# Kernel tuning notes

Measured on AMD Instinct MI355X. Metric: run time of the kernel, lower is better.

The kernel has to match this reference:

```python
import jax, jax.numpy as jnp
import numpy as np
from jax import lax

B, H, W, C = 8, 64, 64, 256  # H must equal W (einsum contraction requires it)
CQ = C // 4


def conv2d(x, w, b, dilation=1):
    # x: NHWC, w: HWIO (TF Conv2D layout), padding 'same'
    y = lax.conv_general_dilated(
        x, w, window_strides=(1, 1), padding='SAME',
        rhs_dilation=(dilation, dilation),
        dimension_numbers=('NHWC', 'HWIO', 'NHWC'))
    return y + b


def setup_inputs() -> dict:
    key = jax.random.key(0)
    ks = jax.random.split(key, 16)
    s = 0.05
    inp = {
        'x':   jax.random.normal(ks[0], (B, H, W, C), jnp.float32),
        'wq':  jax.random.normal(ks[1], (1, 1, C, CQ), jnp.float32) * s,
        'bq':  jnp.zeros((CQ,), jnp.float32),
        'wq1': jax.random.normal(ks[2], (3, 3, C, CQ), jnp.float32) * s,
        'bq1': jnp.zeros((CQ,), jnp.float32),
        'wq2': jax.random.normal(ks[3], (3, 3, C, CQ), jnp.float32) * s,
        'bq2': jnp.zeros((CQ,), jnp.float32),
        'wq3': jax.random.normal(ks[4], (3, 3, C, CQ), jnp.float32) * s,
        'bq3': jnp.zeros((CQ,), jnp.float32),
        'wq4': jax.random.normal(ks[5], (1, 1, C, C), jnp.float32) * s,
        'bq4': jnp.zeros((C,), jnp.float32),
        'wk':  jax.random.normal(ks[6], (3, 3, C, C), jnp.float32) * s,
        'bk':  jnp.zeros((C,), jnp.float32),
        'wv':  jax.random.normal(ks[7], (1, 1, C, C), jnp.float32) * s,
        'bv':  jnp.zeros((C,), jnp.float32),
        'gamma': jax.random.normal(ks[8], (1,), jnp.float32) * 0.1,
    }
    return inp


def reference(x, wq, bq, wq1, bq1, wq2, bq2, wq3, bq3, wq4, bq4,
              wk, bk, wv, bv, gamma):
    # multi-scale query branch: 1x1, 3x3, 3x3 dil=3, 3x3 dil=6 -> concat -> 1x1
    q = jnp.concatenate([
        conv2d(x, wq, bq, 1),
        conv2d(x, wq1, bq1, 1),
        conv2d(x, wq2, bq2, 3),
        conv2d(x, wq3, bq3, 6),
    ], axis=-1)
    q = conv2d(q, wq4, bq4, 1)                 # (B,H,W,C)
    # key conv applied twice with the SAME weights (as in the original code)
    k = conv2d(conv2d(x, wk, bk, 1), wk, bk, 1)  # (B,H,W,C)
    v = conv2d(x, wv, bv, 1)                    # (B,H,W,C)

    qT = jnp.transpose(q, (0, 2, 1, 3))         # (B,W,H,C)
    # per-channel spatial contraction; requires H == W
    energy = jnp.einsum('bijc,bkjc->bikc', k, qT)   # (B,H,W,C)
    attention = jax.nn.softmax(energy, axis=-1)     # softmax over CHANNEL axis
    attnT = jnp.transpose(attention, (0, 2, 1, 3))  # (B,W,H,C)
    out = jnp.einsum('bijc,bkjc->bikc', attnT, v)   # (B,W,H,C)
    return gamma * out + x
```

## Files before the change

kernel.cpp:

```cpp
#include <hip/hip_runtime.h>

typedef short  short8 __attribute__((ext_vector_type(8)));
typedef short  sv4    __attribute__((ext_vector_type(4)));
typedef __bf16 bf16x8 __attribute__((ext_vector_type(8)));
typedef float  f32x4  __attribute__((ext_vector_type(4)));

__device__ __forceinline__ float bf2f(short s) {
    unsigned u = ((unsigned)(unsigned short)s) << 16;
    return __builtin_bit_cast(float, u);
}
__device__ __forceinline__ short f2bf(float f) {
    unsigned u = __builtin_bit_cast(unsigned, f);
    u += 0x7fffu + ((u >> 16) & 1u);
    return (short)(u >> 16);
}
__device__ __forceinline__ f32x4 mfma16(short8 a, short8 b, f32x4 c) {
    return __builtin_amdgcn_mfma_f32_16x16x32_bf16(
        __builtin_bit_cast(bf16x8, a), __builtin_bit_cast(bf16x8, b), c, 0, 0, 0);
}
__device__ __forceinline__ void gl16(const short* g, short* l) {
    __builtin_amdgcn_global_load_lds(
        (const __attribute__((address_space(1))) void*)g,
        (__attribute__((address_space(3))) void*)l, 16, 0, 0);
}


__global__ __launch_bounds__(256) void detect_k(const short* x, int* flag)
{
    __shared__ int red[256];
    int t = threadIdx.x;
    int cnt = 0;
    for (int i = t; i < 4096; i += 256) {
        int e = (x[2 * i] >> 7) & 0xFF;
        cnt += (e >= 100 && e <= 140) ? 1 : 0;
    }
    red[t] = cnt; __syncthreads();
    for (int s = 128; s > 0; s >>= 1) { if (t < s) red[t] += red[t + s]; __syncthreads(); }
    if (t == 0) *flag = (red[0] < 3277) ? 1 : 0;
}

__global__ __launch_bounds__(256) void convert_x(const void* x, short* xb, const int* flagp)
{
    int f32 = *flagp;
    size_t i = ((size_t)blockIdx.x * 256 + threadIdx.x) * 8;
    short8 v;
    if (f32) {
        const float* fs = (const float*)x + i;
        f32x4 a = *(const f32x4*)fs;
        f32x4 b = *(const f32x4*)(fs + 4);
#pragma unroll
        for (int l = 0; l < 4; l++) { v[l] = f2bf(a[l]); v[4 + l] = f2bf(b[l]); }
    } else {
        v = *(const short8*)((const short*)x + i);
    }
    *(short8*)(xb + i) = v;
}

struct Ptrs {
    const void *wq, *wq1, *wq2, *wq3, *wq4, *wk, *wv;
    const void *bq, *bq1, *bq2, *bq3, *bq4, *bk, *bv, *gm;
};

__global__ __launch_bounds__(256) void convert_k(Ptrs P, short* wp, short* bb, const int* flagp)
{
    int f32 = *flagp;
    int bid = blockIdx.x;
    int tid = threadIdx.x;
    if (bid < 288) {
        __shared__ short T[64][66];
        const void* src; int Cout, dbase, lb;
        if      (bid <   4) { src = P.wq;  Cout =  64; dbase = 0;       lb = bid; }
        else if (bid <  40) { src = P.wq1; Cout =  64; dbase = 16384;   lb = bid - 4; }
        else if (bid <  76) { src = P.wq2; Cout =  64; dbase = 163840;  lb = bid - 40; }
        else if (bid < 112) { src = P.wq3; Cout =  64; dbase = 311296;  lb = bid - 76; }
        else if (bid < 128) { src = P.wq4; Cout = 256; dbase = 458752;  lb = bid - 112; }
        else if (bid < 272) { src = P.wk;  Cout = 256; dbase = 524288;  lb = bid - 128; }
        else                { src = P.wv;  Cout = 256; dbase = 1114112; lb = bid - 272; }
        int t, ci0, co0;
        if (Cout == 64) { t = lb >> 2; ci0 = (lb & 3) * 64; co0 = 0; }
        else            { t = lb >> 4; ci0 = ((lb >> 2) & 3) * 64; co0 = (lb & 3) * 64; }
        int rrow = tid >> 6, ccol = tid & 63;
#pragma unroll
        for (int r = 0; r < 16; ++r) {
            int cir = r * 4 + rrow;
            long si = (long)(t * 256 + ci0 + cir) * Cout + co0 + ccol;
            T[cir][ccol] = f32 ? f2bf(((const float*)src)[si]) : ((const short*)src)[si];
        }
        __syncthreads();
#pragma unroll
        for (int r = 0; r < 16; ++r) {
            int cow = r * 4 + rrow;
            wp[dbase + (t * Cout + co0 + cow) * 256 + ci0 + ccol] = T[ccol][cow];
        }
    } else {
        for (int j = tid; j < 1280; j += 256) {
            if (j < 1025) {
                const void* src; int off;
                if      (j <   64) { src = P.bq;  off = j; }
                else if (j <  128) { src = P.bq1; off = j - 64; }
                else if (j <  192) { src = P.bq2; off = j - 128; }
                else if (j <  256) { src = P.bq3; off = j - 192; }
                else if (j <  512) { src = P.bq4; off = j - 256; }
                else if (j <  768) { src = P.bk;  off = j - 512; }
                else if (j < 1024) { src = P.bv;  off = j - 768; }
                else               { src = P.gm;  off = 0; }
                bb[j] = f32 ? f2bf(((const float*)src)[off]) : ((const short*)src)[off];
            } else if (j >= 1032) {
                bb[j] = 0;
            }
        }
    }
}

struct CJob {
    const short* src;
    short*       dst;
    const short* wpk;
    const short* bias;
    int Cout;
    int dil;
    int ntaps;
    int coff;
    int outmode;
};
struct CTable { CJob j[6]; int end[6]; };

template<int NA, int NB, int BOFS, int WSTEP>
__device__ __forceinline__ void conv_loop(
    const short* src, const short* wpk, int ntaps, int dil,
    const short* zp, short* Sh,
    int wave, int lr8, int cl, int h0, int b, int nt0, int srcT,
    int m_base, int n_base, int lrow, int pc0, int pc1,
    f32x4 (&acc)[4][4])
{
    const short* abase[NA];
    unsigned     vm[NA];
    const short* bbase[NB];
#pragma unroll
    for (int jj = 0; jj < NA; jj++) {
        int m  = (jj * 4 + wave) * 8 + lr8;
        int hh = srcT ? (m & 63) : (h0 + (m >> 6));
        int ww = srcT ? (h0 + (m >> 6)) : (m & 63);
        abase[jj] = src + (((b * 64 + hh) * 64 + ww) * 256 + cl * 8);
        unsigned msk = 1u;
        if (ntaps == 9) {
            msk = 0u;
#pragma unroll
            for (int t = 0; t < 9; ++t) {
                int tr = (t >= 6) ? 2 : ((t >= 3) ? 1 : 0);
                int dy = (tr - 1) * dil, dx = (t - tr * 3 - 1) * dil;
                bool v = ((unsigned)(hh + dy) < 64u) && ((unsigned)(ww + dx) < 64u);
                msk |= (v ? 1u : 0u) << t;
            }
        }
        vm[jj] = msk;
    }
#pragma unroll
    for (int jj = 0; jj < NB; jj++) {
        int n = (jj * 4 + wave) * 8 + lr8;
        bbase[jj] = wpk + (nt0 + n) * 256 + cl * 8;
    }

    int prevdel = 0;
    for (int t = 0; t < ntaps; ++t) {
        int dy = 0, dx = 0;
        if (ntaps == 9) {
            int tr = (t >= 6) ? 2 : ((t >= 3) ? 1 : 0);
            dy = (tr - 1) * dil;
            dx = (t - tr * 3 - 1) * dil;
        }
        int tdel = (dy * 64 + dx) * 256;
        int step = tdel - prevdel; prevdel = tdel;
        const short* pA[NA];
#pragma unroll
        for (int jj = 0; jj < NA; jj++) {
            abase[jj] += step;
            pA[jj] = ((vm[jj] >> t) & 1u) ? abase[jj] : zp;
        }
#pragma unroll
        for (int s4 = 0; s4 < 4; ++s4) {
#pragma unroll
            for (int jj = 0; jj < NA; jj++)
                gl16(pA[jj] + s4 * 64, Sh + (jj * 4 + wave) * 512);
#pragma unroll
            for (int jj = 0; jj < NB; jj++)
                gl16(bbase[jj] + s4 * 64, Sh + BOFS + (jj * 4 + wave) * 512);
            __syncthreads();
#pragma unroll
            for (int j = 0; j < 2; j++) {
                int pc = j ? pc1 : pc0;
                short8 a4[4], b4[4];
#pragma unroll
                for (int mi = 0; mi < 4; mi++)
                    a4[mi] = *(const short8*)(Sh + (m_base + mi * 16 + lrow) * 64 + pc);
#pragma unroll
                for (int ni = 0; ni < 4; ni++)
                    b4[ni] = *(const short8*)(Sh + BOFS + (n_base + ni * 16 + lrow) * 64 + pc);
#pragma unroll
                for (int mi = 0; mi < 4; mi++)
#pragma unroll
                    for (int ni = 0; ni < 4; ni++)
                        acc[mi][ni] = mfma16(a4[mi], b4[ni], acc[mi][ni]);
            }
            __syncthreads();
        }
#pragma unroll
        for (int jj = 0; jj < NB; jj++) bbase[jj] += WSTEP;
    }
}

__global__ __launch_bounds__(256, 3) void conv_tile(CTable T, const short* zp)
{
    __shared__ short Sh[20480];
    int tid = threadIdx.x;
    int bid = blockIdx.x;
    int ji = 0;
    while (ji < 5 && bid >= T.end[ji]) ji++;
    CJob J = T.j[ji];
    int s0  = ji ? T.end[ji - 1] : 0;
    int seg = T.end[ji] - s0;
    int lb  = bid - s0;
    int g   = (lb & 7) * (seg >> 3) + (lb >> 3);

    int big   = (J.Cout == 256);
    int BM    = big ? 128 : 256;
    int ntile = big ? (g & 1) : 0;
    int Mtile = big ? (g >> 1) : g;
    int p0 = Mtile * BM;
    int b  = p0 >> 12;
    int h0 = (p0 >> 6) & 63;
    int nt0  = ntile * 128;
    int srcT = (J.outmode == 3);

    int wave = tid >> 6, lane = tid & 63;
    int lrow = lane & 15, quad = lane >> 4;
    int m_base = big ? (wave & 1) * 64 : wave * 64;
    int n_base = big ? (wave >> 1) * 64 : 0;

    int lr8 = lane >> 3;
    int cl  = (lane & 7) ^ (lr8 & 7);

    int pc0 = ((quad     ^ (lrow & 7)) * 8);
    int pc1 = (((4 + quad) ^ (lrow & 7)) * 8);

    f32x4 acc[4][4] = {};
    if (big)
        conv_loop<4, 4, 8192, 65536>(J.src, J.wpk, J.ntaps, J.dil, zp, Sh,
                                     wave, lr8, cl, h0, b, nt0, srcT,
                                     m_base, n_base, lrow, pc0, pc1, acc);
    else
        conv_loop<8, 2, 16384, 16384>(J.src, J.wpk, J.ntaps, J.dil, zp, Sh,
                                      wave, lr8, cl, h0, b, nt0, srcT,
                                      m_base, n_base, lrow, pc0, pc1, acc);

    int rq = quad * 4;
#pragma unroll
    for (int ni = 0; ni < 4; ni++) {
        int co = nt0 + n_base + ni * 16 + lrow;
        float bv = bf2f(J.bias[co]);
        if (J.outmode == 0) {
#pragma unroll
            for (int mi = 0; mi < 4; mi++) {
                int pb = p0 + m_base + mi * 16 + rq;
#pragma unroll
                for (int r = 0; r < 4; r++)
                    J.dst[(size_t)(pb + r) * 256 + J.coff + co] = f2bf(acc[mi][ni][r] + bv);
            }
        } else {
            int hw = h0 + (m_base >> 6);
            short* row = J.dst + ((size_t)(b * 256 + co) * 64 + hw) * 64;
#pragma unroll
            for (int mi = 0; mi < 4; mi++) {
                sv4 o;
#pragma unroll
                for (int r = 0; r < 4; r++) o[r] = f2bf(acc[mi][ni][r] + bv);
                *(sv4*)(row + mi * 16 + rq) = o;
            }
        }
    }
}

__global__ __launch_bounds__(256) void energy_mfma(const short* qp, const short* kp, float* Et)
{
    int wid  = threadIdx.x >> 6;
    int lane = threadIdx.x & 63;
    int g = blockIdx.x * 4 + wid;
    int b = g >> 8, c = g & 255;
    int lrow = lane & 15;
    int q8   = (lane >> 4) << 3;
    const short* qb = qp + (size_t)(b * 256 + c) * 4096;
    const short* kb = kp + (size_t)(b * 256 + c) * 4096;

    f32x4 acc[4][4] = {};
#pragma unroll
    for (int ks = 0; ks < 2; ++ks) {
        int j0 = ks * 32 + q8;
        short8 A[4], Bv[4];
#pragma unroll
        for (int mi = 0; mi < 4; mi++)
            A[mi] = *(const short8*)(qb + (size_t)(mi * 16 + lrow) * 64 + j0);
#pragma unroll
        for (int ni = 0; ni < 4; ni++)
            Bv[ni] = *(const short8*)(kb + (size_t)(ni * 16 + lrow) * 64 + j0);
#pragma unroll
        for (int mi = 0; mi < 4; mi++)
#pragma unroll
            for (int ni = 0; ni < 4; ni++)
                acc[mi][ni] = mfma16(A[mi], Bv[ni], acc[mi][ni]);
    }
    int rq = (lane >> 4) * 4;
#pragma unroll
    for (int mi = 0; mi < 4; mi++)
#pragma unroll
        for (int r = 0; r < 4; r++) {
            int w = mi * 16 + rq + r;
            float* row = Et + ((size_t)(b * 256 + c) * 64 + w) * 64;
#pragma unroll
            for (int ni = 0; ni < 4; ni++)
                row[ni * 16 + lrow] = acc[mi][ni][r];
        }
}

__global__ __launch_bounds__(256) void softmax_k(const float* Et, short* att)
{
    __shared__ float S[256 * 33];
    __shared__ float red[256];
    __shared__ float sm[256];
    int t  = threadIdx.x;
    int b  = blockIdx.x >> 7;
    int a  = (blockIdx.x >> 1) & 63;
    int jh = blockIdx.x & 1;

    const float* row = Et + ((size_t)(b * 256 + t) * 64 + a) * 64 + jh * 32;
#pragma unroll
    for (int jj = 0; jj < 32; jj += 4) {
        f32x4 v = *(const f32x4*)(row + jj);
#pragma unroll
        for (int l = 0; l < 4; l++) S[t * 33 + jj + l] = v[l];
    }
    __syncthreads();

    int tj = t & 31, tg = t >> 5;
    float m = -1e30f;
#pragma unroll
    for (int cc = 0; cc < 32; ++cc) m = fmaxf(m, S[(tg * 32 + cc) * 33 + tj]);
    red[t] = m;
    __syncthreads();
    if (tg == 0) {
        float mm = red[tj];
#pragma unroll
        for (int gg = 1; gg < 8; ++gg) mm = fmaxf(mm, red[gg * 32 + tj]);
        red[tj] = mm;
    }
    __syncthreads();
    float M = red[tj];
    float s = 0.f;
#pragma unroll
    for (int cc = 0; cc < 32; ++cc) {
        int id = (tg * 32 + cc) * 33 + tj;
        float e = __expf(S[id] - M);
        S[id] = e; s += e;
    }
    sm[t] = s;
    __syncthreads();
    if (tg == 0) {
        float ss = sm[tj];
#pragma unroll
        for (int gg = 1; gg < 8; ++gg) ss += sm[gg * 32 + tj];
        sm[tj] = 1.0f / ss;
    }
    __syncthreads();

    short* orow = att + ((size_t)(b * 256 + t) * 64 + a) * 64 + jh * 32;
#pragma unroll
    for (int jj = 0; jj < 32; jj += 8) {
        short8 o;
#pragma unroll
        for (int l = 0; l < 8; l++) o[l] = f2bf(S[t * 33 + jj + l] * sm[jj + l]);
        *(short8*)(orow + jj) = o;
    }
}

__global__ __launch_bounds__(512) void out_final(const short* vp, const short* att,
                                                 const void* x, const void* gamma,
                                                 void* out, const int* flagp)
{
    __shared__ float S[8 * 16 * 66];
    int f32 = *flagp;
    int tid = threadIdx.x;
    int wid = tid >> 6, lane = tid & 63;
    int b  = blockIdx.x & 7;
    int c0 = (blockIdx.x >> 3) * 8;
    int c  = c0 + wid;
    int lrow = lane & 15, quad = lane >> 4;
    int q8 = quad << 3;
    const short* vb = vp  + (size_t)(b * 256 + c) * 4096;
    const short* ab = att + (size_t)(b * 256 + c) * 4096;

    f32x4 acc[4][4] = {};
#pragma unroll
    for (int ks = 0; ks < 2; ++ks) {
        int j0 = ks * 32 + q8;
        short8 A[4], Bv[4];
#pragma unroll
        for (int mi = 0; mi < 4; mi++)
            A[mi] = *(const short8*)(vb + (size_t)(mi * 16 + lrow) * 64 + j0);
#pragma unroll
        for (int ni = 0; ni < 4; ni++)
            Bv[ni] = *(const short8*)(ab + (size_t)(ni * 16 + lrow) * 64 + j0);
#pragma unroll
        for (int mi = 0; mi < 4; mi++)
#pragma unroll
            for (int ni = 0; ni < 4; ni++)
                acc[mi][ni] = mfma16(A[mi], Bv[ni], acc[mi][ni]);
    }

    float gm = f32 ? ((const float*)gamma)[0] : bf2f(((const short*)gamma)[0]);
    int rq = quad * 4;
#pragma unroll
    for (int mi = 0; mi < 4; mi++) {
#pragma unroll
        for (int ni = 0; ni < 4; ni++)
#pragma unroll
            for (int r = 0; r < 4; r++)
                S[(wid * 16 + rq + r) * 66 + ni * 16 + lrow] = acc[mi][ni][r];
        __syncthreads();
#pragma unroll
        for (int it = 0; it < 2; ++it) {
            int idx = it * 512 + tid;
            int dp = idx >> 6;
            int p  = idx & 63;
            int dg = mi * 16 + dp;
            size_t off = ((size_t)((b * 64 + p) * 64 + dg)) * 256 + c0;
            if (f32) {
                const float* xs = (const float*)x + off;
                float* os = (float*)out + off;
                f32x4 xv0 = *(const f32x4*)xs;
                f32x4 xv1 = *(const f32x4*)(xs + 4);
                f32x4 o0, o1;
#pragma unroll
                for (int l = 0; l < 4; l++) {
                    o0[l] = gm * S[((l    ) * 16 + dp) * 66 + p] + xv0[l];
                    o1[l] = gm * S[((l + 4) * 16 + dp) * 66 + p] + xv1[l];
                }
                *(f32x4*)os = o0;
                *(f32x4*)(os + 4) = o1;
            } else {
                const short* xs = (const short*)x + off;
                short* os = (short*)out + off;
                short8 xv = *(const short8*)xs, o;
#pragma unroll
                for (int l = 0; l < 8; l++)
                    o[l] = f2bf(gm * S[(l * 16 + dp) * 66 + p] + bf2f(xv[l]));
                *(short8*)os = o;
            }
        }
        __syncthreads();
    }
}

extern "C" void kernel_launch(void* const* d_in, const int* in_sizes, int n_in,
                              void* d_out, int out_size, void* d_ws, size_t ws_size,
                              hipStream_t stream)
{
    const void* x   = d_in[0];
    Ptrs P{ d_in[1], d_in[3], d_in[5], d_in[7], d_in[9], d_in[11], d_in[13],
            d_in[2], d_in[4], d_in[6], d_in[8], d_in[10], d_in[12], d_in[14], d_in[15] };

    short* ws   = (short*)d_ws;
    short* qcat = ws;
    short* k1   = ws + 8388608;
    short* qp   = ws + 16777216;
    short* kp   = ws + 25165824;
    short* vp   = ws + 33554432;
    short* wp   = ws + 41943040;
    short* bb   = ws + 43122688;
    int*   flag = (int*)(ws + 43123968);
    short* xb   = qp;
    float* Et   = (float*)d_ws;
    short* att  = qp;
    const short* zp = bb + 1032;

    detect_k<<<1, 256, 0, stream>>>((const short*)x, flag);
    convert_x<<<4096, 256, 0, stream>>>(x, xb, flag);
    convert_k<<<289, 256, 0, stream>>>(P, wp, bb, flag);

    CJob j4{ xb, k1,   wp + 524288,  bb + 512, 256, 1, 9, 0,   0 };
    CJob j1{ xb, qcat, wp + 16384,   bb + 64,  64,  1, 9, 64,  0 };
    CJob j2{ xb, qcat, wp + 163840,  bb + 128, 64,  3, 9, 128, 0 };
    CJob j3{ xb, qcat, wp + 311296,  bb + 192, 64,  6, 9, 192, 0 };
    CJob jb{ xb, vp,   wp + 1114112, bb + 768, 256, 1, 1, 0,   2 };
    CJob ja{ xb, qcat, wp + 0,       bb + 0,   64,  1, 1, 0,   0 };
    CTable TA{ { j4, j1, j2, j3, jb, ja }, { 512, 640, 768, 896, 1408, 1536 } };
    conv_tile<<<1536, 256, 0, stream>>>(TA, zp);

    CJob j6{ k1,   kp, wp + 524288, bb + 512, 256, 1, 9, 0, 2 };
    CJob j5{ qcat, qp, wp + 458752, bb + 256, 256, 1, 1, 0, 3 };
    CTable TB{ { j6, j5, j5, j5, j5, j5 }, { 512, 1024, 1024, 1024, 1024, 1024 } };
    conv_tile<<<1024, 256, 0, stream>>>(TB, zp);

    energy_mfma<<<512, 256, 0, stream>>>(qp, kp, Et);
    softmax_k<<<1024, 256, 0, stream>>>(Et, att);
    out_final<<<256, 512, 0, stream>>>(vp, att, x, d_in[15], d_out, flag);
}
```

Baseline: 314.0 us.

## Shrink small-conv tiles to raise occupancy and store energy in bf16

Splits the templated conv loop into separate big and small variants. The small Cout=64 jobs now use 128-row M tiles instead of 256, which doubles their block count, cuts shared memory to 32KB and raises launch bounds to 4 blocks per CU. The energy matrix is now written and read as bf16 instead of fp32, halving that intermediate's memory traffic. The cost is lower precision in the softmax input, plus more blocks that each reload their weights.

New measurement: 1.133 ms. 3.61x slower.

```diff
diff --git a/kernel.cpp b/kernel.cpp
--- a/kernel.cpp
+++ b/kernel.cpp
@@ -125,23 +125,21 @@
 };
 struct CTable { CJob j[6]; int end[6]; };
 
-template<int NA, int NB, int BOFS, int WSTEP>
-__device__ __forceinline__ void conv_loop(
+__device__ __forceinline__ void conv_big_loop(
     const short* src, const short* wpk, int ntaps, int dil,
     const short* zp, short* Sh,
     int wave, int lr8, int cl, int h0, int b, int nt0, int srcT,
     int m_base, int n_base, int lrow, int pc0, int pc1,
     f32x4 (&acc)[4][4])
 {
-    const short* abase[NA];
-    unsigned     vm[NA];
-    const short* bbase[NB];
-#pragma unroll
-    for (int jj = 0; jj < NA; jj++) {
-        int m  = (jj * 4 + wave) * 8 + lr8;
+    const short* aroot[4];
+    unsigned     vm[4];
+#pragma unroll
+    for (int jj = 0; jj < 4; jj++) {
+        int m  = jj * 32 + wave * 8 + lr8;
         int hh = srcT ? (m & 63) : (h0 + (m >> 6));
         int ww = srcT ? (h0 + (m >> 6)) : (m & 63);
-        abase[jj] = src + (((b * 64 + hh) * 64 + ww) * 256 + cl * 8);
+        aroot[jj] = src + (((b * 64 + hh) * 64 + ww) * 256 + cl * 8);
         unsigned msk = 1u;
         if (ntaps == 9) {
             msk = 0u;
@@ -155,11 +153,7 @@
         }
         vm[jj] = msk;
     }
-#pragma unroll
-    for (int jj = 0; jj < NB; jj++) {
-        int n = (jj * 4 + wave) * 8 + lr8;
-        bbase[jj] = wpk + (nt0 + n) * 256 + cl * 8;
-    }
+    const short* broot = wpk + (nt0 + wave * 8 + lr8) * 256 + cl * 8;
 
     int prevdel = 0;
     for (int t = 0; t < ntaps; ++t) {
@@ -171,20 +165,20 @@
         }
         int tdel = (dy * 64 + dx) * 256;
         int step = tdel - prevdel; prevdel = tdel;
-        const short* pA[NA];
-#pragma unroll
-        for (int jj = 0; jj < NA; jj++) {
-            abase[jj] += step;
-            pA[jj] = ((vm[jj] >> t) & 1u) ? abase[jj] : zp;
+        const short* pA[4];
+#pragma unroll
+        for (int jj = 0; jj < 4; jj++) {
+            aroot[jj] += step;
+            pA[jj] = ((vm[jj] >> t) & 1u) ? aroot[jj] : zp;
         }
 #pragma unroll
         for (int s4 = 0; s4 < 4; ++s4) {
 #pragma unroll
-            for (int jj = 0; jj < NA; jj++)
+            for (int jj = 0; jj < 4; jj++)
                 gl16(pA[jj] + s4 * 64, Sh + (jj * 4 + wave) * 512);
 #pragma unroll
-            for (int jj = 0; jj < NB; jj++)
-                gl16(bbase[jj] + s4 * 64, Sh + BOFS + (jj * 4 + wave) * 512);
+            for (int jj = 0; jj < 4; jj++)
+                gl16(broot + jj * 8192 + s4 * 64, Sh + 8192 + (jj * 4 + wave) * 512);
             __syncthreads();
 #pragma unroll
             for (int j = 0; j < 2; j++) {
@@ -195,7 +189,7 @@
                     a4[mi] = *(const short8*)(Sh + (m_base + mi * 16 + lrow) * 64 + pc);
 #pragma unroll
                 for (int ni = 0; ni < 4; ni++)
-                    b4[ni] = *(const short8*)(Sh + BOFS + (n_base + ni * 16 + lrow) * 64 + pc);
+                    b4[ni] = *(const short8*)(Sh + 8192 + (n_base + ni * 16 + lrow) * 64 + pc);
 #pragma unroll
                 for (int mi = 0; mi < 4; mi++)
 #pragma unroll
@@ -204,14 +198,96 @@
             }
             __syncthreads();
         }
-#pragma unroll
-        for (int jj = 0; jj < NB; jj++) bbase[jj] += WSTEP;
-    }
-}
-
-__global__ __launch_bounds__(256, 3) void conv_tile(CTable T, const short* zp)
-{
-    __shared__ short Sh[20480];
+        broot += 65536;
+    }
+}
+
+__device__ __forceinline__ void conv_small_loop(
+    const short* src, const short* wpk, int ntaps, int dil,
+    const short* zp, short* Sh,
+    int wave, int lr8, int cl, int h0, int b,
+    int m_base, int n_base, int lrow, int pc0, int pc1,
+    f32x4 (&acc)[4][4])
+{
+    const short* abase[4];
+    unsigned     vm[4];
+    const short* bbase[2];
+#pragma unroll
+    for (int jj = 0; jj < 4; jj++) {
+        int m  = (jj * 4 + wave) * 8 + lr8;
+        int hh = h0 + (m >> 6);
+        int ww = m & 63;
+        abase[jj] = src + (((b * 64 + hh) * 64 + ww) * 256 + cl * 8);
+        unsigned msk = 1u;
+        if (ntaps == 9) {
+            msk = 0u;
+#pragma unroll
+            for (int t = 0; t < 9; ++t) {
+                int tr = (t >= 6) ? 2 : ((t >= 3) ? 1 : 0);
+                int dy = (tr - 1) * dil, dx = (t - tr * 3 - 1) * dil;
+                bool v = ((unsigned)(hh + dy) < 64u) && ((unsigned)(ww + dx) < 64u);
+                msk |= (v ? 1u : 0u) << t;
+            }
+        }
+        vm[jj] = msk;
+    }
+#pragma unroll
+    for (int jj = 0; jj < 2; jj++) {
+        int n = (jj * 4 + wave) * 8 + lr8;
+        bbase[jj] = wpk + n * 256 + cl * 8;
+    }
+
+    int prevdel = 0;
+    for (int t = 0; t < ntaps; ++t) {
+        int dy = 0, dx = 0;
+        if (ntaps == 9) {
+            int tr = (t >= 6) ? 2 : ((t >= 3) ? 1 : 0);
+            dy = (tr - 1) * dil;
+            dx = (t - tr * 3 - 1) * dil;
+        }
+        int tdel = (dy * 64 + dx) * 256;
+        int step = tdel - prevdel; prevdel = tdel;
+        const short* pA[4];
+#pragma unroll
+        for (int jj = 0; jj < 4; jj++) {
+            abase[jj] += step;
+            pA[jj] = ((vm[jj] >> t) & 1u) ? abase[jj] : zp;
+        }
+#pragma unroll
+        for (int s4 = 0; s4 < 4; ++s4) {
+#pragma unroll
+            for (int jj = 0; jj < 4; jj++)
+                gl16(pA[jj] + s4 * 64, Sh + (jj * 4 + wave) * 512);
+#pragma unroll
+            for (int jj = 0; jj < 2; jj++)
+                gl16(bbase[jj] + s4 * 64, Sh + 8192 + (jj * 4 + wave) * 512);
+            __syncthreads();
+#pragma unroll
+            for (int j = 0; j < 2; j++) {
+                int pc = j ? pc1 : pc0;
+                short8 a4[2], b4[4];
+#pragma unroll
+                for (int mi = 0; mi < 2; mi++)
+                    a4[mi] = *(const short8*)(Sh + (m_base + mi * 16 + lrow) * 64 + pc);
+#pragma unroll
+                for (int ni = 0; ni < 4; ni++)
+                    b4[ni] = *(const short8*)(Sh + 8192 + (n_base + ni * 16 + lrow) * 64 + pc);
+#pragma unroll
+                for (int mi = 0; mi < 2; mi++)
+#pragma unroll
+                    for (int ni = 0; ni < 4; ni++)
+                        acc[mi][ni] = mfma16(a4[mi], b4[ni], acc[mi][ni]);
+            }
+            __syncthreads();
+        }
+#pragma unroll
+        for (int jj = 0; jj < 2; jj++) bbase[jj] += 16384;
+    }
+}
+
+__global__ __launch_bounds__(256, 4) void conv2(CTable T, const short* zp)
+{
+    __shared__ short Sh[16384];
     int tid = threadIdx.x;
     int bid = blockIdx.x;
     int ji = 0;
@@ -223,10 +299,9 @@
     int g   = (lb & 7) * (seg >> 3) + (lb >> 3);
 
     int big   = (J.Cout == 256);
-    int BM    = big ? 128 : 256;
     int ntile = big ? (g & 1) : 0;
     int Mtile = big ? (g >> 1) : g;
-    int p0 = Mtile * BM;
+    int p0 = Mtile * 128;
     int b  = p0 >> 12;
     int h0 = (p0 >> 6) & 63;
     int nt0  = ntile * 128;
@@ -234,7 +309,7 @@
 
     int wave = tid >> 6, lane = tid & 63;
     int lrow = lane & 15, quad = lane >> 4;
-    int m_base = big ? (wave & 1) * 64 : wave * 64;
+    int m_base = big ? (wave & 1) * 64 : wave * 32;
     int n_base = big ? (wave >> 1) * 64 : 0;
 
     int lr8 = lane >> 3;
@@ -245,42 +320,43 @@
 
     f32x4 acc[4][4] = {};
     if (big)
-        conv_loop<4, 4, 8192, 65536>(J.src, J.wpk, J.ntaps, J.dil, zp, Sh,
-                                     wave, lr8, cl, h0, b, nt0, srcT,
-                                     m_base, n_base, lrow, pc0, pc1, acc);
+        conv_big_loop(J.src, J.wpk, J.ntaps, J.dil, zp, Sh,
+                      wave, lr8, cl, h0, b, nt0, srcT,
+                      m_base, n_base, lrow, pc0, pc1, acc);
     else
-        conv_loop<8, 2, 16384, 16384>(J.src, J.wpk, J.ntaps, J.dil, zp, Sh,
-                                      wave, lr8, cl, h0, b, nt0, srcT,
-                                      m_base, n_base, lrow, pc0, pc1, acc);
+        conv_small_loop(J.src, J.wpk, J.ntaps, J.dil, zp, Sh,
+                        wave, lr8, cl, h0, b,
+                        m_base, n_base, lrow, pc0, pc1, acc);
 
     int rq = quad * 4;
+    int MI = big ? 4 : 2;
 #pragma unroll
     for (int ni = 0; ni < 4; ni++) {
         int co = nt0 + n_base + ni * 16 + lrow;
         float bv = bf2f(J.bias[co]);
         if (J.outmode == 0) {
-#pragma unroll
-            for (int mi = 0; mi < 4; mi++) {
+            for (int mi = 0; mi < MI; mi++) {
                 int pb = p0 + m_base + mi * 16 + rq;
 #pragma unroll
                 for (int r = 0; r < 4; r++)
                     J.dst[(size_t)(pb + r) * 256 + J.coff + co] = f2bf(acc[mi][ni][r] + bv);
             }
         } else {
-            int hw = h0 + (m_base >> 6);
-            short* row = J.dst + ((size_t)(b * 256 + co) * 64 + hw) * 64;
 #pragma unroll
             for (int mi = 0; mi < 4; mi++) {
+                int mb = m_base + mi * 16;
+                int hw = h0 + (mb >> 6);
+                short* row = J.dst + ((size_t)(b * 256 + co) * 64 + hw) * 64;
                 sv4 o;
 #pragma unroll
                 for (int r = 0; r < 4; r++) o[r] = f2bf(acc[mi][ni][r] + bv);
-                *(sv4*)(row + mi * 16 + rq) = o;
-            }
-        }
-    }
-}
-
-__global__ __launch_bounds__(256) void energy_mfma(const short* qp, const short* kp, float* Et)
+                *(sv4*)(row + ((mb + rq) & 63)) = o;
+            }
+        }
+    }
+}
+
+__global__ __launch_bounds__(256) void energy_mfma(const short* qp, const short* kp, short* Et)
 {
     int wid  = threadIdx.x >> 6;
     int lane = threadIdx.x & 63;
@@ -314,14 +390,14 @@
 #pragma unroll
         for (int r = 0; r < 4; r++) {
             int w = mi * 16 + rq + r;
-            float* row = Et + ((size_t)(b * 256 + c) * 64 + w) * 64;
+            short* row = Et + ((size_t)(b * 256 + c) * 64 + w) * 64;
 #pragma unroll
             for (int ni = 0; ni < 4; ni++)
-                row[ni * 16 + lrow] = acc[mi][ni][r];
-        }
-}
-
-__global__ __launch_bounds__(256) void softmax_k(const float* Et, short* att)
+                row[ni * 16 + lrow] = f2bf(acc[mi][ni][r]);
+        }
+}
+
+__global__ __launch_bounds__(256) void softmax_k(const short* Et, short* att)
 {
     __shared__ float S[256 * 33];
     __shared__ float red[256];
@@ -331,12 +407,12 @@
     int a  = (blockIdx.x >> 1) & 63;
     int jh = blockIdx.x & 1;
 
-    const float* row = Et + ((size_t)(b * 256 + t) * 64 + a) * 64 + jh * 32;
-#pragma unroll
-    for (int jj = 0; jj < 32; jj += 4) {
-        f32x4 v = *(const f32x4*)(row + jj);
-#pragma unroll
-        for (int l = 0; l < 4; l++) S[t * 33 + jj + l] = v[l];
+    const short* row = Et + ((size_t)(b * 256 + t) * 64 + a) * 64 + jh * 32;
+#pragma unroll
+    for (int jj = 0; jj < 32; jj += 8) {
+        short8 v = *(const short8*)(row + jj);
+#pragma unroll
+        for (int l = 0; l < 8; l++) S[t * 33 + jj + l] = bf2f(v[l]);
     }
     __syncthreads();
 
@@ -477,7 +553,7 @@
     short* bb   = ws + 43122688;
     int*   flag = (int*)(ws + 43123968);
     short* xb   = qp;
-    float* Et   = (float*)d_ws;
+    short* Et   = ws;
     short* att  = qp;
     const short* zp = bb + 1032;
 
@@ -491,13 +567,13 @@
     CJob j3{ xb, qcat, wp + 311296,  bb + 192, 64,  6, 9, 192, 0 };
     CJob jb{ xb, vp,   wp + 1114112, bb + 768, 256, 1, 1, 0,   2 };
     CJob ja{ xb, qcat, wp + 0,       bb + 0,   64,  1, 1, 0,   0 };
-    CTable TA{ { j4, j1, j2, j3, jb, ja }, { 512, 640, 768, 896, 1408, 1536 } };
-    conv_tile<<<1536, 256, 0, stream>>>(TA, zp);
+    CTable TA{ { j4, j1, j2, j3, jb, ja }, { 512, 768, 1024, 1280, 1792, 2048 } };
+    conv2<<<2048, 256, 0, stream>>>(TA, zp);
 
     CJob j6{ k1,   kp, wp + 524288, bb + 512, 256, 1, 9, 0, 2 };
     CJob j5{ qcat, qp, wp + 458752, bb + 256, 256, 1, 1, 0, 3 };
     CTable TB{ { j6, j5, j5, j5, j5, j5 }, { 512, 1024, 1024, 1024, 1024, 1024 } };
-    conv_tile<<<1024, 256, 0, stream>>>(TB, zp);
+    conv2<<<1024, 256, 0, stream>>>(TB, zp);
 
     energy_mfma<<<512, 256, 0, stream>>>(qp, kp, Et);
     softmax_k<<<1024, 256, 0, stream>>>(Et, att);
```
